# Optimization experiments

Hardware: AMD Instinct MI355X
Metric: run time of the kernel (lower is better)

Reference implementation:

```python
import jax, jax.numpy as jnp
import numpy as np


def _squash_global(v):
    # Faithful to torch: v.norm() with no dim -> global Frobenius norm (scalar).
    n2 = jnp.sum(v * v)
    n = jnp.sqrt(n2)
    scale = n2 / (1.0 + n2)
    return scale * v / n


def setup_inputs() -> dict:
    key = jax.random.key(0)
    k1, k2 = jax.random.split(key)
    B, R, Ci = 128, 1152, 8
    C, O = 10, 16
    x = jax.random.normal(k1, (B, R, Ci), dtype=jnp.float32)
    W = jax.random.normal(k2, (C, R, Ci, O), dtype=jnp.float32)  # routing_weights ~ randn
    return {"x": x, "W": W, "num_iterations": 3}


def reference(x, W, num_iterations):
    # prediction_vectors: [C, B, R, 1, O]
    u = jnp.einsum('bri,crio->cbro', x, W)[:, :, :, None, :]
    logits = jnp.zeros_like(u)
    v = None
    for _ in range(num_iterations):
        # batch_softmax: cat over dim0 + legacy softmax(dim=1 of 4D) == softmax over
        # the num_route_nodes axis (axis 2 here).
        c = jax.nn.softmax(logits, axis=2)
        s = jnp.sum(c * u, axis=2, keepdims=True)  # [C, B, 1, 1, O]
        v = _squash_global(s)
        logits = logits + u * v
    return v
```

## Files before the change

kernel.cpp:

```cpp
#include <hip/hip_runtime.h>
#include <math.h>

#define Bn   128
#define Rn   1152
#define CIn  8
#define Cn   10
#define On   16
#define BO   2048
#define CBO  20480
#define RC   12
#define NSEG 96
#define PSEG 24

__global__ __launch_bounds__(256)
void transpose_x(const float* __restrict__ X, float* __restrict__ XT)
{
    const int r = blockIdx.x;
    const int b = threadIdx.x & 127;
    const int g = threadIdx.x >> 7;
    float4 v = *(const float4*)(X + (size_t)b * (Rn * CIn) + r * CIn + g * 4);
    ((float4*)XT)[r * 256 + g * 128 + b] = v;
}

template<int PASS>
__global__ __launch_bounds__(256, 2)
void pass_kernel(const float* __restrict__ XT, const float* __restrict__ W,
                 const float* __restrict__ Sprev, const float* __restrict__ N2,
                 float* __restrict__ PT, float* __restrict__ PL)
{
    __shared__ float red[4][64][34];

    const int blk  = blockIdx.x;
    const int c    = blk / 48;
    const int rem  = blk - c * 48;
    const int bh   = rem / 24;
    const int segq = rem - bh * 24;
    const int tid  = threadIdx.x;
    const int w    = tid >> 6;
    const int lane = tid & 63;
    const int b    = bh * 64 + lane;
    const int r0   = __builtin_amdgcn_readfirstlane((segq * 4 + w) * RC);

    float vs[16];
    if (PASS > 1) {
        float coef[PASS];
        #pragma unroll
        for (int t = 0; t < PASS - 1; ++t) {
            const float n2 = N2[t];
            coef[t] = n2 / ((1.0f + n2) * sqrtf(n2)) * 1.4426950408889634f;
        }
        const float* sp = Sprev + c * BO + b * On;
        #pragma unroll
        for (int q = 0; q < 4; ++q) {
            float4 a = make_float4(0.f, 0.f, 0.f, 0.f);
            #pragma unroll
            for (int t = 0; t < PASS - 1; ++t) {
                const float4 s4 = *(const float4*)(sp + t * CBO + q * 4);
                a.x = fmaf(coef[t], s4.x, a.x);
                a.y = fmaf(coef[t], s4.y, a.y);
                a.z = fmaf(coef[t], s4.z, a.z);
                a.w = fmaf(coef[t], s4.w, a.w);
            }
            vs[q * 4 + 0] = a.x; vs[q * 4 + 1] = a.y;
            vs[q * 4 + 2] = a.z; vs[q * 4 + 3] = a.w;
        }
    }

    float tacc[16], lacc[16];
    #pragma unroll
    for (int o = 0; o < 16; ++o) { tacc[o] = 0.0f; lacc[o] = 0.0f; }

    const float4* XT4 = (const float4*)XT;
    for (int rr = 0; rr < RC; ++rr) {
        const int r = r0 + rr;
        const float4 xa = XT4[r * 256 + b];
        const float4 xb = XT4[r * 256 + 128 + b];
        const int woff = __builtin_amdgcn_readfirstlane((c * Rn + r) * 128);
        const float* wr = W + woff;
        #pragma unroll
        for (int o = 0; o < 16; ++o) {
            float u = xa.x * wr[o];
            u = fmaf(xa.y, wr[16 + o], u);
            u = fmaf(xa.z, wr[32 + o], u);
            u = fmaf(xa.w, wr[48 + o], u);
            u = fmaf(xb.x, wr[64 + o], u);
            u = fmaf(xb.y, wr[80 + o], u);
            u = fmaf(xb.z, wr[96 + o], u);
            u = fmaf(xb.w, wr[112 + o], u);
            if (PASS == 1) {
                tacc[o] += u;
            } else {
                const float e = exp2f(u * vs[o]);
                lacc[o] += e;
                tacc[o] = fmaf(e, u, tacc[o]);
            }
        }
    }

    #pragma unroll
    for (int o = 0; o < 16; ++o) {
        red[w][lane][o]      = tacc[o];
        red[w][lane][16 + o] = lacc[o];
    }
    __syncthreads();

    {
        const int bl = tid >> 2;
        const int og = tid & 3;
        const int bg = bh * 64 + bl;
        float4 tv, lv;
        float* tp = (float*)&tv;
        float* lp = (float*)&lv;
        #pragma unroll
        for (int q = 0; q < 4; ++q) {
            const int o = og * 4 + q;
            tp[q] = red[0][bl][o] + red[1][bl][o] + red[2][bl][o] + red[3][bl][o];
            lp[q] = red[0][bl][16 + o] + red[1][bl][16 + o] +
                    red[2][bl][16 + o] + red[3][bl][16 + o];
        }
        const int idx = segq * CBO + c * BO + bg * On + og * 4;
        *(float4*)(PT + idx) = tv;
        if (PASS > 1) *(float4*)(PL + idx) = lv;
    }
}

template<int PASS>
__global__ __launch_bounds__(256)
void combine_kernel(const float* __restrict__ PT, const float* __restrict__ PL,
                    float* __restrict__ Sout, float* __restrict__ n2out)
{
    const int i = blockIdx.x * 256 + threadIdx.x;
    float T = 0.0f, L = 0.0f;
    #pragma unroll
    for (int s = 0; s < PSEG; ++s) T += PT[s * CBO + i];
    if (PASS == 1) {
        L = (float)Rn;
    } else {
        #pragma unroll
        for (int s = 0; s < PSEG; ++s) L += PL[s * CBO + i];
    }
    const float sv = T / L;
    Sout[i] = sv;
    float sq = sv * sv;
    #pragma unroll
    for (int d = 1; d < 64; d <<= 1) sq += __shfl_xor(sq, d);
    __shared__ float red[4];
    if ((threadIdx.x & 63) == 0) red[threadIdx.x >> 6] = sq;
    __syncthreads();
    if (threadIdx.x == 0)
        atomicAdd(n2out, red[0] + red[1] + red[2] + red[3]);
}

__global__ __launch_bounds__(256)
void final_kernel(const float* __restrict__ S, const float* __restrict__ n2p,
                  float* __restrict__ out)
{
    const int i = blockIdx.x * 256 + threadIdx.x;
    const float n2 = *n2p;
    const float coef = n2 / ((1.0f + n2) * sqrtf(n2));
    out[i] = coef * S[i];
}

extern "C" void kernel_launch(void* const* d_in, const int* in_sizes, int n_in,
                              void* d_out, int out_size, void* d_ws, size_t ws_size,
                              hipStream_t stream)
{
    const float* X = (const float*)d_in[0];
    const float* W = (const float*)d_in[1];
    float* ws = (float*)d_ws;
    float* XT = ws;
    float* N2 = XT + Rn * Bn * CIn;
    float* PT = N2 + 4;
    float* PL = PT + PSEG * CBO;
    float* S  = PL + PSEG * CBO;

    hipMemsetAsync(N2, 0, 16, stream);

    transpose_x<<<Rn, 256, 0, stream>>>(X, XT);
    pass_kernel<1><<<480, 256, 0, stream>>>(XT, W, S, N2, PT, PL);
    combine_kernel<1><<<80, 256, 0, stream>>>(PT, PL, S + 0 * CBO, N2 + 0);
    pass_kernel<2><<<480, 256, 0, stream>>>(XT, W, S, N2, PT, PL);
    combine_kernel<2><<<80, 256, 0, stream>>>(PT, PL, S + 1 * CBO, N2 + 1);
    pass_kernel<3><<<480, 256, 0, stream>>>(XT, W, S, N2, PT, PL);
    combine_kernel<3><<<80, 256, 0, stream>>>(PT, PL, S + 2 * CBO, N2 + 2);
    final_kernel<<<80, 256, 0, stream>>>(S + 2 * CBO, N2 + 2, (float*)d_out);
}
```

Before: 124.5 us.

## Retile pass kernel so each lane computes 4 outputs for 4 batch rows

Each lane previously owned one batch row and all 16 outputs, reading W through scalar (wave-uniform) loads. Now a lane owns 4 outputs (og) across 4 batch rows, loading W as per-lane float4 vectors and reusing each across 4 batches. The grid grows to 720 blocks with 72 route segments of 16 routes, split into two 8-route halves reduced through a smaller LDS buffer, and occupancy is raised to 3 blocks per CU. This aims for more parallelism and cheaper reduction, but it triples the partial-sum traffic that combine_kernel must read and makes W loads vector rather than scalar.

```diff
diff --git a/kernel.cpp b/kernel.cpp
--- a/kernel.cpp
+++ b/kernel.cpp
@@ -8,9 +8,12 @@
 #define On   16
 #define BO   2048
 #define CBO  20480
-#define RC   12
-#define NSEG 96
-#define PSEG 24
+#define PSEG 72
+#define LSTR 20
+
+#define F4SET0(a)      a.x=0.f; a.y=0.f; a.z=0.f; a.w=0.f
+#define F4FMA(acc,s,v) acc.x=fmaf(s,v.x,acc.x); acc.y=fmaf(s,v.y,acc.y); \
+                       acc.z=fmaf(s,v.z,acc.z); acc.w=fmaf(s,v.w,acc.w)
 
 __global__ __launch_bounds__(256)
 void transpose_x(const float* __restrict__ X, float* __restrict__ XT)
@@ -23,25 +26,27 @@
 }
 
 template<int PASS>
-__global__ __launch_bounds__(256, 2)
+__global__ __launch_bounds__(256, 3)
 void pass_kernel(const float* __restrict__ XT, const float* __restrict__ W,
                  const float* __restrict__ Sprev, const float* __restrict__ N2,
                  float* __restrict__ PT, float* __restrict__ PL)
 {
-    __shared__ float red[4][64][34];
+    __shared__ float ldsT[2][64 * LSTR];
+    __shared__ float ldsL[2][64 * LSTR];
 
     const int blk  = blockIdx.x;
-    const int c    = blk / 48;
-    const int rem  = blk - c * 48;
-    const int bh   = rem / 24;
-    const int segq = rem - bh * 24;
+    const int c    = blk / PSEG;
+    const int segq = blk - c * PSEG;
     const int tid  = threadIdx.x;
-    const int w    = tid >> 6;
+    const int wv   = tid >> 6;
+    const int bh   = wv & 1;
+    const int rsub = wv >> 1;
     const int lane = tid & 63;
-    const int b    = bh * 64 + lane;
-    const int r0   = __builtin_amdgcn_readfirstlane((segq * 4 + w) * RC);
-
-    float vs[16];
+    const int bq   = lane & 15;
+    const int og   = lane >> 4;
+    const int r0   = segq * 16 + rsub * 8;
+
+    float4 vs[4];
     if (PASS > 1) {
         float coef[PASS];
         #pragma unroll
@@ -49,78 +54,97 @@
             const float n2 = N2[t];
             coef[t] = n2 / ((1.0f + n2) * sqrtf(n2)) * 1.4426950408889634f;
         }
-        const float* sp = Sprev + c * BO + b * On;
-        #pragma unroll
-        for (int q = 0; q < 4; ++q) {
-            float4 a = make_float4(0.f, 0.f, 0.f, 0.f);
+        #pragma unroll
+        for (int j = 0; j < 4; ++j) {
+            const int b = bh * 64 + j * 16 + bq;
+            float4 a; F4SET0(a);
             #pragma unroll
             for (int t = 0; t < PASS - 1; ++t) {
-                const float4 s4 = *(const float4*)(sp + t * CBO + q * 4);
-                a.x = fmaf(coef[t], s4.x, a.x);
-                a.y = fmaf(coef[t], s4.y, a.y);
-                a.z = fmaf(coef[t], s4.z, a.z);
-                a.w = fmaf(coef[t], s4.w, a.w);
+                const float4 s4 = *(const float4*)(Sprev + t * CBO + c * BO + b * On + og * 4);
+                F4FMA(a, coef[t], s4);
             }
-            vs[q * 4 + 0] = a.x; vs[q * 4 + 1] = a.y;
-            vs[q * 4 + 2] = a.z; vs[q * 4 + 3] = a.w;
-        }
-    }
-
-    float tacc[16], lacc[16];
-    #pragma unroll
-    for (int o = 0; o < 16; ++o) { tacc[o] = 0.0f; lacc[o] = 0.0f; }
+            vs[j] = a;
+        }
+    }
+
+    float4 tacc[4], lacc[4];
+    #pragma unroll
+    for (int j = 0; j < 4; ++j) { F4SET0(tacc[j]); F4SET0(lacc[j]); }
 
     const float4* XT4 = (const float4*)XT;
-    for (int rr = 0; rr < RC; ++rr) {
+    const float*  wc  = W + (size_t)c * Rn * 128;
+
+    #pragma unroll
+    for (int rr = 0; rr < 8; ++rr) {
         const int r = r0 + rr;
-        const float4 xa = XT4[r * 256 + b];
-        const float4 xb = XT4[r * 256 + 128 + b];
-        const int woff = __builtin_amdgcn_readfirstlane((c * Rn + r) * 128);
-        const float* wr = W + woff;
-        #pragma unroll
-        for (int o = 0; o < 16; ++o) {
-            float u = xa.x * wr[o];
-            u = fmaf(xa.y, wr[16 + o], u);
-            u = fmaf(xa.z, wr[32 + o], u);
-            u = fmaf(xa.w, wr[48 + o], u);
-            u = fmaf(xb.x, wr[64 + o], u);
-            u = fmaf(xb.y, wr[80 + o], u);
-            u = fmaf(xb.z, wr[96 + o], u);
-            u = fmaf(xb.w, wr[112 + o], u);
+        float4 wf[8];
+        #pragma unroll
+        for (int i = 0; i < 8; ++i)
+            wf[i] = *(const float4*)(wc + r * 128 + i * On + og * 4);
+        float4 xa[4], xb[4];
+        #pragma unroll
+        for (int j = 0; j < 4; ++j) {
+            const int b = bh * 64 + j * 16 + bq;
+            xa[j] = XT4[r * 256 + b];
+            xb[j] = XT4[r * 256 + 128 + b];
+        }
+        #pragma unroll
+        for (int j = 0; j < 4; ++j) {
+            float4 u;
+            u.x = xa[j].x * wf[0].x; u.y = xa[j].x * wf[0].y;
+            u.z = xa[j].x * wf[0].z; u.w = xa[j].x * wf[0].w;
+            F4FMA(u, xa[j].y, wf[1]);
+            F4FMA(u, xa[j].z, wf[2]);
+            F4FMA(u, xa[j].w, wf[3]);
+            F4FMA(u, xb[j].x, wf[4]);
+            F4FMA(u, xb[j].y, wf[5]);
+            F4FMA(u, xb[j].z, wf[6]);
+            F4FMA(u, xb[j].w, wf[7]);
             if (PASS == 1) {
-                tacc[o] += u;
+                tacc[j].x += u.x; tacc[j].y += u.y;
+                tacc[j].z += u.z; tacc[j].w += u.w;
             } else {
-                const float e = exp2f(u * vs[o]);
-                lacc[o] += e;
-                tacc[o] = fmaf(e, u, tacc[o]);
+                float4 e;
+                e.x = exp2f(u.x * vs[j].x);
+                e.y = exp2f(u.y * vs[j].y);
+                e.z = exp2f(u.z * vs[j].z);
+                e.w = exp2f(u.w * vs[j].w);
+                lacc[j].x += e.x; lacc[j].y += e.y;
+                lacc[j].z += e.z; lacc[j].w += e.w;
+                tacc[j].x = fmaf(e.x, u.x, tacc[j].x);
+                tacc[j].y = fmaf(e.y, u.y, tacc[j].y);
+                tacc[j].z = fmaf(e.z, u.z, tacc[j].z);
+                tacc[j].w = fmaf(e.w, u.w, tacc[j].w);
             }
         }
     }
 
-    #pragma unroll
-    for (int o = 0; o < 16; ++o) {
-        red[w][lane][o]      = tacc[o];
-        red[w][lane][16 + o] = lacc[o];
+    if (rsub == 1) {
+        #pragma unroll
+        for (int j = 0; j < 4; ++j) {
+            const int row = (j * 16 + bq) * LSTR + og * 4;
+            *(float4*)&ldsT[bh][row] = tacc[j];
+            if (PASS > 1) *(float4*)&ldsL[bh][row] = lacc[j];
+        }
     }
     __syncthreads();
-
-    {
-        const int bl = tid >> 2;
-        const int og = tid & 3;
-        const int bg = bh * 64 + bl;
-        float4 tv, lv;
-        float* tp = (float*)&tv;
-        float* lp = (float*)&lv;
-        #pragma unroll
-        for (int q = 0; q < 4; ++q) {
-            const int o = og * 4 + q;
-            tp[q] = red[0][bl][o] + red[1][bl][o] + red[2][bl][o] + red[3][bl][o];
-            lp[q] = red[0][bl][16 + o] + red[1][bl][16 + o] +
-                    red[2][bl][16 + o] + red[3][bl][16 + o];
-        }
-        const int idx = segq * CBO + c * BO + bg * On + og * 4;
-        *(float4*)(PT + idx) = tv;
-        if (PASS > 1) *(float4*)(PL + idx) = lv;
+    if (rsub == 0) {
+        #pragma unroll
+        for (int j = 0; j < 4; ++j) {
+            const int row = (j * 16 + bq) * LSTR + og * 4;
+            const float4 ot = *(const float4*)&ldsT[bh][row];
+            tacc[j].x += ot.x; tacc[j].y += ot.y;
+            tacc[j].z += ot.z; tacc[j].w += ot.w;
+            const int b   = bh * 64 + j * 16 + bq;
+            const int idx = segq * CBO + c * BO + b * On + og * 4;
+            *(float4*)(PT + idx) = tacc[j];
+            if (PASS > 1) {
+                const float4 ol = *(const float4*)&ldsL[bh][row];
+                lacc[j].x += ol.x; lacc[j].y += ol.y;
+                lacc[j].z += ol.z; lacc[j].w += ol.w;
+                *(float4*)(PL + idx) = lacc[j];
+            }
+        }
     }
 }
 
@@ -177,11 +201,11 @@
     hipMemsetAsync(N2, 0, 16, stream);
 
     transpose_x<<<Rn, 256, 0, stream>>>(X, XT);
-    pass_kernel<1><<<480, 256, 0, stream>>>(XT, W, S, N2, PT, PL);
+    pass_kernel<1><<<720, 256, 0, stream>>>(XT, W, S, N2, PT, PL);
     combine_kernel<1><<<80, 256, 0, stream>>>(PT, PL, S + 0 * CBO, N2 + 0);
-    pass_kernel<2><<<480, 256, 0, stream>>>(XT, W, S, N2, PT, PL);
+    pass_kernel<2><<<720, 256, 0, stream>>>(XT, W, S, N2, PT, PL);
     combine_kernel<2><<<80, 256, 0, stream>>>(PT, PL, S + 1 * CBO, N2 + 1);
-    pass_kernel<3><<<480, 256, 0, stream>>>(XT, W, S, N2, PT, PL);
+    pass_kernel<3><<<720, 256, 0, stream>>>(XT, W, S, N2, PT, PL);
     combine_kernel<3><<<80, 256, 0, stream>>>(PT, PL, S + 2 * CBO, N2 + 2);
     final_kernel<<<80, 256, 0, stream>>>(S + 2 * CBO, N2 + 2, (float*)d_out);
 }
```

New measurement: 195.0 us. 1.57x slower.
